# Optimization experiments

Hardware: AMD Instinct MI355X
Metric: run time of the kernel (lower is better)

The kernel has to match this reference:

```python
import jax, jax.numpy as jnp
import numpy as np

D_IN = 1024
D_OUT = 1024
NUM_HEADS = 16
HEAD_DIM = D_OUT // NUM_HEADS


def setup_inputs() -> dict:
    key = jax.random.key(0)
    kx, kq, kk, kv, ko = jax.random.split(key, 5)
    s = 1.0 / np.sqrt(D_IN)
    return {
        "x": jax.random.normal(kx, (1, 4096, D_IN), dtype=jnp.float32),
        "Wq": jax.random.normal(kq, (D_IN, D_OUT), dtype=jnp.float32) * s,
        "Wk": jax.random.normal(kk, (D_IN, D_OUT), dtype=jnp.float32) * s,
        "Wv": jax.random.normal(kv, (D_IN, D_OUT), dtype=jnp.float32) * s,
        "Wo": jax.random.normal(ko, (D_OUT, D_OUT), dtype=jnp.float32) * s,
    }


def reference(x, Wq, Wk, Wv, Wo):
    b, s, _ = x.shape
    # project and split heads: [b, h, s, d]
    def split_heads(t):
        return t.reshape(b, s, NUM_HEADS, HEAD_DIM).transpose(0, 2, 1, 3)
    Q = split_heads(x @ Wq)
    K = split_heads(x @ Wk)
    V = split_heads(x @ Wv)
    scores = jnp.einsum("bhqd,bhkd->bhqk", Q, K) / jnp.sqrt(jnp.float32(HEAD_DIM))
    causal = jnp.triu(jnp.ones((s, s), dtype=bool), k=1)  # True above diagonal
    scores = jnp.where(causal, -jnp.inf, scores)
    probs = jax.nn.softmax(scores, axis=-1)
    out = jnp.einsum("bhqk,bhkd->bhqd", probs, V)
    out = out.transpose(0, 2, 1, 3).reshape(b, s, D_OUT)
    return out @ Wo
```

## Files before the change

kernel.cpp:

```cpp
#include <hip/hip_runtime.h>
#include <cstdint>

#define S_LEN 4096
#define D_MODEL 1024
#define NHEAD 16
#define HDIM 64

typedef __bf16 bf16_t;
typedef __bf16 bf16x8 __attribute__((ext_vector_type(8)));
typedef __bf16 bf16x4 __attribute__((ext_vector_type(4)));
typedef float floatx4 __attribute__((ext_vector_type(4)));

#define QSCALE 0.18033688011112042f

__device__ __forceinline__ void lds_cp16(void* lds, const void* g) {
    __builtin_amdgcn_global_load_lds(
        (const __attribute__((address_space(1))) unsigned int*)g,
        (__attribute__((address_space(3))) unsigned int*)lds,
        16, 0, 0);
}

__device__ __forceinline__ float fast_exp2(float x) {
    float r;
    asm("v_exp_f32 %0, %1" : "=v"(r) : "v"(x));
    return r;
}

__global__ __launch_bounds__(256) void k_prep(const float* __restrict__ x,
                                              const float* __restrict__ Wq,
                                              const float* __restrict__ Wk,
                                              const float* __restrict__ Wv,
                                              const float* __restrict__ Wo,
                                              bf16_t* __restrict__ xb,
                                              bf16_t* __restrict__ WtQKV,
                                              bf16_t* __restrict__ WtO) {
    const int bx = blockIdx.x;
    if (bx < 4096) {
        int i = bx * 256 + threadIdx.x;
        float4 v = ((const float4*)x)[i];
        bf16x4 o;
        o[0] = (bf16_t)v.x; o[1] = (bf16_t)v.y; o[2] = (bf16_t)v.z; o[3] = (bf16_t)v.w;
        *(bf16x4*)(xb + (size_t)i * 4) = o;
        return;
    }
    __shared__ float lds[64][65];
    const int i = bx - 4096;
    const int z = i >> 8, rem = i & 255;
    const float* W = (z == 0) ? Wq : (z == 1) ? Wk : (z == 2) ? Wv : Wo;
    bf16_t* Wt = (z < 3) ? (WtQKV + (size_t)z * 1048576) : WtO;
    const int k0 = (rem >> 4) * 64, n0 = (rem & 15) * 64;
    const int t = threadIdx.x, cl = t & 63, rl = t >> 6;
#pragma unroll
    for (int r = 0; r < 16; ++r)
        lds[r * 4 + rl][cl] = W[(size_t)(k0 + r * 4 + rl) * 1024 + n0 + cl];
    __syncthreads();
#pragma unroll
    for (int r = 0; r < 16; ++r)
        Wt[(size_t)(n0 + r * 4 + rl) * 1024 + k0 + cl] = (bf16_t)lds[cl][r * 4 + rl];
}

template <int MODE, int MT>
__global__ __launch_bounds__(256) void k_gemm(const bf16_t* __restrict__ A,
                                              const bf16_t* __restrict__ Bt,
                                              float* __restrict__ Cout,
                                              bf16_t* __restrict__ Qb,
                                              bf16_t* __restrict__ Kb,
                                              bf16_t* __restrict__ Vt) {
    constexpr int MI = MT / 32;
    __shared__ __align__(16) bf16_t sA[MT * 32];
    __shared__ __align__(16) bf16_t sB[128 * 32];
    const int t = threadIdx.x, w = t >> 6, lane = t & 63, quad = lane >> 4, l15 = lane & 15;
    const int m0 = blockIdx.x * MT, n0 = blockIdx.y * 128;
    const int wm = w >> 1, wn = w & 1;

    floatx4 acc[MI][4];
#pragma unroll
    for (int i = 0; i < MI; ++i)
#pragma unroll
        for (int j = 0; j < 4; ++j)
            acc[i][j] = floatx4{0.f, 0.f, 0.f, 0.f};

    for (int kb = 0; kb < 32; ++kb) {
        __syncthreads();
#pragma unroll
        for (int r = 0; r < MT / 64; ++r) {
            int c = t + 256 * r;
            int row = c >> 2, kq = c & 3;
            lds_cp16(&sA[w * 512 + r * 2048],
                     A + (size_t)(m0 + row) * 1024 + kb * 32 + kq * 8);
        }
#pragma unroll
        for (int r = 0; r < 2; ++r) {
            int c = t + 256 * r;
            int row = c >> 2, kq = c & 3;
            lds_cp16(&sB[w * 512 + r * 2048],
                     Bt + (size_t)(n0 + row) * 1024 + kb * 32 + kq * 8);
        }
        __syncthreads();
        bf16x8 af[MI], bfr[4];
#pragma unroll
        for (int i = 0; i < MI; ++i)
            af[i] = *(const bf16x8*)&sA[(wm * (MT / 2) + i * 16 + l15) * 32 + quad * 8];
#pragma unroll
        for (int j = 0; j < 4; ++j)
            bfr[j] = *(const bf16x8*)&sB[(wn * 64 + j * 16 + l15) * 32 + quad * 8];
#pragma unroll
        for (int i = 0; i < MI; ++i)
#pragma unroll
            for (int j = 0; j < 4; ++j)
                acc[i][j] = __builtin_amdgcn_mfma_f32_16x16x32_bf16(af[i], bfr[j],
                                                                    acc[i][j], 0, 0, 0);
    }

    const int mrow = m0 + wm * (MT / 2) + quad * 4;
    if (MODE == 0) {
        const int ncol = n0 + wn * 64 + l15;
#pragma unroll
        for (int i = 0; i < MI; ++i)
#pragma unroll
            for (int j = 0; j < 4; ++j)
#pragma unroll
                for (int r = 0; r < 4; ++r)
                    Cout[(size_t)(mrow + i * 16 + r) * 1024 + ncol + j * 16] = acc[i][j][r];
    } else {
        const int g = (int)blockIdx.y >> 3;
        const int ncbase = ((int)blockIdx.y & 7) * 128 + wn * 64 + l15;
        if (g == 2) {
#pragma unroll
            for (int j = 0; j < 4; ++j) {
                int nc = ncbase + j * 16;
                int hh = nc >> 6, dd = nc & 63;
                bf16_t* dst = Vt + (size_t)hh * 262144 + (size_t)dd * 64;
#pragma unroll
                for (int i = 0; i < MI; ++i) {
                    int s0r = mrow + i * 16;
                    bf16x4 pk;
                    pk[0] = (bf16_t)acc[i][j][0]; pk[1] = (bf16_t)acc[i][j][1];
                    pk[2] = (bf16_t)acc[i][j][2]; pk[3] = (bf16_t)acc[i][j][3];
                    int kk = s0r & 63;
                    int pp = (kk & 0x20) | ((kk & 0xC) << 1) | ((kk & 0x10) >> 2);
                    *(bf16x4*)&dst[(size_t)(s0r >> 6) * 4096 + pp] = pk;
                }
            }
        } else {
            bf16_t* base = g ? Kb : Qb;
            const float sc = g ? 1.0f : QSCALE;
#pragma unroll
            for (int j = 0; j < 4; ++j) {
                int nc = ncbase + j * 16;
                int hh = nc >> 6, dd = nc & 63;
#pragma unroll
                for (int i = 0; i < MI; ++i)
#pragma unroll
                    for (int r = 0; r < 4; ++r)
                        base[(size_t)hh * 262144 + (size_t)(mrow + i * 16 + r) * 64 + dd] =
                            (bf16_t)(acc[i][j][r] * sc);
            }
        }
    }
}

__global__ __launch_bounds__(256, 4) void k_attn(const bf16_t* __restrict__ Qb,
                                                 const bf16_t* __restrict__ Kb,
                                                 const bf16_t* __restrict__ Vt,
                                                 bf16_t* __restrict__ OP0,
                                                 bf16_t* __restrict__ OP1,
                                                 float* __restrict__ Lp) {
    __shared__ __align__(16) bf16_t Ks[2][64 * 64];
    __shared__ __align__(16) bf16_t Vts[2][64 * 64];
    const int bid = blockIdx.x;
    const int slot = bid >> 8, jj = bid & 255, g = jj >> 5, u = jj & 31;
    const int h = u >> 1, sp = u & 1;
    const int qb = (slot == 0) ? (31 - g) : (slot == 1) ? (16 + g)
                 : (slot == 2) ? (15 - g) : g;
    const int t = threadIdx.x, w = t >> 6, quad = (t & 63) >> 4, l15 = t & 15;
    const bf16_t* Qh = Qb + (size_t)h * 262144;
    const bf16_t* Kh = Kb + (size_t)h * 262144;
    const bf16_t* Vth = Vt + (size_t)h * 262144;

    const bf16_t* Qrow = Qh + (size_t)(qb * 128 + w * 32 + l15) * 64;
    bf16x8 bq[2][2];
#pragma unroll
    for (int qt = 0; qt < 2; ++qt)
#pragma unroll
        for (int kh = 0; kh < 2; ++kh)
            bq[qt][kh] = *(const bf16x8*)(Qrow + qt * 1024 + kh * 32 + quad * 8);

    bf16x8 vones;
#pragma unroll
    for (int e = 0; e < 8; ++e) vones[e] = (bf16_t)1.0f;

    floatx4 lacc[2];
    floatx4 o_acc[2][4];
#pragma unroll
    for (int qt = 0; qt < 2; ++qt) {
        lacc[qt] = floatx4{0.f, 0.f, 0.f, 0.f};
#pragma unroll
        for (int j = 0; j < 4; ++j) o_acc[qt][j] = floatx4{0.f, 0.f, 0.f, 0.f};
    }

#define STAGE_K(b, kb_)                                                            \
    {                                                                              \
        _Pragma("unroll") for (int r = 0; r < 2; ++r) {                            \
            int c = t + 256 * r;                                                   \
            int row = c >> 3, sw = (c & 7) ^ (row & 7);                            \
            lds_cp16(&Ks[b][c * 8], Kh + (size_t)(kb_) * 4096 + row * 64 + sw * 8);\
        }                                                                          \
    }
#define STAGE_V(b, kb_)                                                            \
    {                                                                              \
        _Pragma("unroll") for (int r = 0; r < 2; ++r) {                            \
            int c = t + 256 * r;                                                   \
            int row = c >> 3, sw = (c & 7) ^ (row & 7);                            \
            lds_cp16(&Vts[b][c * 8], Vth + (size_t)(kb_) * 4096 + row * 64 + sw * 8);\
        }                                                                          \
    }

    const int t0 = sp ? (qb + 1) : 0;
    const int nIter = qb + 1;
    const int qmax = qb * 128 + w * 32 + 31;

    STAGE_K(0, t0)
    STAGE_V(0, t0)
    for (int it = 0; it < nIter; ++it) {
        const int kb = t0 + it;
        const int buf = it & 1;
        __syncthreads();
        if (it + 1 < nIter) {
            STAGE_K(buf ^ 1, kb + 1)
            STAGE_V(buf ^ 1, kb + 1)
        }
        const bool active = (kb * 64 <= qmax);

        if (active) {
            floatx4 st[2][4];
            __builtin_amdgcn_s_setprio(1);
#pragma unroll
            for (int j = 0; j < 4; ++j) {
                int rk = j * 16 + l15;
                bf16x8 a0 = *(const bf16x8*)&Ks[buf][rk * 64 + ((quad ^ (rk & 7)) * 8)];
                bf16x8 a1 = *(const bf16x8*)&Ks[buf][rk * 64 + (((quad + 4) ^ (rk & 7)) * 8)];
#pragma unroll
                for (int qt = 0; qt < 2; ++qt) {
                    floatx4 z = {0.f, 0.f, 0.f, 0.f};
                    st[qt][j] = __builtin_amdgcn_mfma_f32_16x16x32_bf16(a0, bq[qt][0], z, 0, 0, 0);
                    st[qt][j] = __builtin_amdgcn_mfma_f32_16x16x32_bf16(a1, bq[qt][1], st[qt][j], 0, 0, 0);
                }
            }
            __builtin_amdgcn_s_setprio(0);
            if (kb >= 2 * qb) {
#pragma unroll
                for (int qt = 0; qt < 2; ++qt) {
                    int qg = qb * 128 + w * 32 + qt * 16 + l15;
#pragma unroll
                    for (int j = 0; j < 4; ++j)
#pragma unroll
                        for (int r = 0; r < 4; ++r) {
                            int keyg = kb * 64 + j * 16 + quad * 4 + r;
                            if (keyg > qg) st[qt][j][r] = -1e30f;
                        }
                }
            }
            bf16x8 pa[2][2];
#pragma unroll
            for (int qt = 0; qt < 2; ++qt) {
#pragma unroll
                for (int j = 0; j < 4; ++j) {
                    st[qt][j][0] = fast_exp2(st[qt][j][0]);
                    st[qt][j][1] = fast_exp2(st[qt][j][1]);
                    st[qt][j][2] = fast_exp2(st[qt][j][2]);
                    st[qt][j][3] = fast_exp2(st[qt][j][3]);
                }
#pragma unroll
                for (int kh = 0; kh < 2; ++kh)
#pragma unroll
                    for (int m = 0; m < 4; ++m) {
                        pa[qt][kh][m]     = (bf16_t)st[qt][2 * kh][m];
                        pa[qt][kh][4 + m] = (bf16_t)st[qt][2 * kh + 1][m];
                    }
            }
            __builtin_amdgcn_s_setprio(1);
#pragma unroll
            for (int kh = 0; kh < 2; ++kh) {
                int pc = kh * 4 + quad;
#pragma unroll
                for (int j = 0; j < 4; ++j) {
                    int rd = j * 16 + l15;
                    bf16x8 bv = *(const bf16x8*)&Vts[buf][rd * 64 + ((pc ^ (rd & 7)) * 8)];
                    o_acc[0][j] = __builtin_amdgcn_mfma_f32_16x16x32_bf16(pa[0][kh], bv, o_acc[0][j], 0, 0, 0);
                    o_acc[1][j] = __builtin_amdgcn_mfma_f32_16x16x32_bf16(pa[1][kh], bv, o_acc[1][j], 0, 0, 0);
                }
                lacc[0] = __builtin_amdgcn_mfma_f32_16x16x32_bf16(pa[0][kh], vones, lacc[0], 0, 0, 0);
                lacc[1] = __builtin_amdgcn_mfma_f32_16x16x32_bf16(pa[1][kh], vones, lacc[1], 0, 0, 0);
            }
            __builtin_amdgcn_s_setprio(0);
        }
    }
    bf16_t* OPx = sp ? OP1 : OP0;
#pragma unroll
    for (int qt = 0; qt < 2; ++qt) {
        if (l15 == 0)
            *(floatx4*)&Lp[sp * 65536 + h * 4096 + qb * 128 + w * 32 + qt * 16 + quad * 4] =
                lacc[qt];
#pragma unroll
        for (int r = 0; r < 4; ++r) {
            int rowg = qb * 128 + w * 32 + qt * 16 + quad * 4 + r;
#pragma unroll
            for (int j = 0; j < 4; ++j)
                OPx[(size_t)rowg * 1024 + h * 64 + j * 16 + l15] = (bf16_t)o_acc[qt][j][r];
        }
    }
#undef STAGE_K
#undef STAGE_V
}

__global__ __launch_bounds__(256) void k_combine(const bf16_t* __restrict__ OP0,
                                                 const bf16_t* __restrict__ OP1,
                                                 const float* __restrict__ Lp,
                                                 bf16_t* __restrict__ Ob) {
    int gi = (blockIdx.x * 256 + threadIdx.x) * 4;
    int q = gi >> 10, hh = (gi & 1023) >> 6;
    float inv = 1.0f / (Lp[hh * 4096 + q] + Lp[65536 + hh * 4096 + q]);
    bf16x4 a = *(const bf16x4*)(OP0 + gi);
    bf16x4 b = *(const bf16x4*)(OP1 + gi);
    bf16x4 o;
#pragma unroll
    for (int r = 0; r < 4; ++r)
        o[r] = (bf16_t)(((float)a[r] + (float)b[r]) * inv);
    *(bf16x4*)(Ob + gi) = o;
}

extern "C" void kernel_launch(void* const* d_in, const int* in_sizes, int n_in,
                              void* d_out, int out_size, void* d_ws, size_t ws_size,
                              hipStream_t stream) {
    const float* x  = (const float*)d_in[0];
    const float* Wq = (const float*)d_in[1];
    const float* Wk = (const float*)d_in[2];
    const float* Wv = (const float*)d_in[3];
    const float* Wo = (const float*)d_in[4];

    bf16_t* ws = (bf16_t*)d_ws;
    bf16_t* Xb    = ws;
    bf16_t* WtQKV = Xb + 4194304;
    bf16_t* WtO   = WtQKV + 3145728;
    bf16_t* Qb    = WtO + 1048576;
    bf16_t* Kb    = Qb + 4194304;
    bf16_t* Vt    = Kb + 4194304;
    bf16_t* Ob    = Vt + 4194304;
    bf16_t* OP1   = Ob + 4194304;
    bf16_t* OP0   = Xb;
    float*  Lp    = (float*)WtQKV;
    float* out = (float*)d_out;

    k_prep<<<5120, 256, 0, stream>>>(x, Wq, Wk, Wv, Wo, Xb, WtQKV, WtO);
    k_gemm<1, 128><<<dim3(32, 24), 256, 0, stream>>>(Xb, WtQKV, nullptr, Qb, Kb, Vt);
    k_attn<<<1024, 256, 0, stream>>>(Qb, Kb, Vt, OP0, OP1, Lp);
    k_combine<<<4096, 256, 0, stream>>>(OP0, OP1, Lp, Ob);
    k_gemm<0, 64><<<dim3(64, 8), 256, 0, stream>>>(Ob, WtO, out, nullptr, nullptr, nullptr);
}
```

Measured before the change: 180.7 us.

## Split long causal query blocks into three KV chunks for better load balance

Reworks the causal attention work split so that the longer query blocks (qb>=16) are divided into three key-range partitions instead of two. Short blocks are packed via lookup tables into two extra slots, and the grid grows from 1024 to 1280 blocks. A third partial-output buffer and row-sum set are written, and the combine kernel adds them for the upper half of rows. The aim is to even out per-block work and reduce tail imbalance, at the cost of more partial-output traffic and extra combine reads.

```diff
diff --git a/kernel.cpp b/kernel.cpp
--- a/kernel.cpp
+++ b/kernel.cpp
@@ -165,14 +165,37 @@
                                                  const bf16_t* __restrict__ Vt,
                                                  bf16_t* __restrict__ OP0,
                                                  bf16_t* __restrict__ OP1,
+                                                 bf16_t* __restrict__ OP2,
                                                  float* __restrict__ Lp) {
     __shared__ __align__(16) bf16_t Ks[2][64 * 64];
     __shared__ __align__(16) bf16_t Vts[2][64 * 64];
     const int bid = blockIdx.x;
-    const int slot = bid >> 8, jj = bid & 255, g = jj >> 5, u = jj & 31;
-    const int h = u >> 1, sp = u & 1;
-    const int qb = (slot == 0) ? (31 - g) : (slot == 1) ? (16 + g)
-                 : (slot == 2) ? (15 - g) : g;
+    const int slot = bid >> 8, jj = bid & 255;
+    const int u = jj & 31, h = u >> 1;
+    const int gp = ((jj >> 5) << 1) | (u & 1);
+
+    int qb, part, c0, c1;
+    if (slot == 0) {
+        qb = 31 - gp; part = 0;
+        c0 = 0; c1 = (2 * qb + 4) / 3;
+    } else if (slot <= 2) {
+        qb = 16 + gp;
+        int L = 2 * qb + 2, p0 = (L + 2) / 3, p1 = (L - p0 + 1) / 2;
+        part = slot;
+        c0 = (slot == 1) ? p0 : p0 + p1;
+        c1 = (slot == 1) ? p0 + p1 : L;
+    } else {
+        if (slot == 3) {
+            qb = (int)((0xaabb77ccdd99eeffULL >> (4 * gp)) & 15);
+            part = gp & 1;
+        } else {
+            qb = (int)((0x0101662323884545ULL >> (4 * gp)) & 15);
+            part = (0xCB2C >> gp) & 1;
+        }
+        c0 = part ? (qb + 1) : 0;
+        c1 = part ? (2 * qb + 2) : (qb + 1);
+    }
+
     const int t = threadIdx.x, w = t >> 6, quad = (t & 63) >> 4, l15 = t & 15;
     const bf16_t* Qh = Qb + (size_t)h * 262144;
     const bf16_t* Kh = Kb + (size_t)h * 262144;
@@ -216,14 +239,13 @@
         }                                                                          \
     }
 
-    const int t0 = sp ? (qb + 1) : 0;
-    const int nIter = qb + 1;
+    const int nIter = c1 - c0;
     const int qmax = qb * 128 + w * 32 + 31;
 
-    STAGE_K(0, t0)
-    STAGE_V(0, t0)
+    STAGE_K(0, c0)
+    STAGE_V(0, c0)
     for (int it = 0; it < nIter; ++it) {
-        const int kb = t0 + it;
+        const int kb = c0 + it;
         const int buf = it & 1;
         __syncthreads();
         if (it + 1 < nIter) {
@@ -296,18 +318,20 @@
             __builtin_amdgcn_s_setprio(0);
         }
     }
-    bf16_t* OPx = sp ? OP1 : OP0;
+    bf16_t* OPx = (part == 0) ? OP0 : (part == 1) ? OP1 : OP2;
+    const int rsub = (part == 2) ? 2048 : 0;
 #pragma unroll
     for (int qt = 0; qt < 2; ++qt) {
         if (l15 == 0)
-            *(floatx4*)&Lp[sp * 65536 + h * 4096 + qb * 128 + w * 32 + qt * 16 + quad * 4] =
+            *(floatx4*)&Lp[part * 65536 + h * 4096 + qb * 128 + w * 32 + qt * 16 + quad * 4] =
                 lacc[qt];
 #pragma unroll
         for (int r = 0; r < 4; ++r) {
             int rowg = qb * 128 + w * 32 + qt * 16 + quad * 4 + r;
 #pragma unroll
             for (int j = 0; j < 4; ++j)
-                OPx[(size_t)rowg * 1024 + h * 64 + j * 16 + l15] = (bf16_t)o_acc[qt][j][r];
+                OPx[(size_t)(rowg - rsub) * 1024 + h * 64 + j * 16 + l15] =
+                    (bf16_t)o_acc[qt][j][r];
         }
     }
 #undef STAGE_K
@@ -316,17 +340,26 @@
 
 __global__ __launch_bounds__(256) void k_combine(const bf16_t* __restrict__ OP0,
                                                  const bf16_t* __restrict__ OP1,
+                                                 const bf16_t* __restrict__ OP2,
                                                  const float* __restrict__ Lp,
                                                  bf16_t* __restrict__ Ob) {
     int gi = (blockIdx.x * 256 + threadIdx.x) * 4;
     int q = gi >> 10, hh = (gi & 1023) >> 6;
-    float inv = 1.0f / (Lp[hh * 4096 + q] + Lp[65536 + hh * 4096 + q]);
+    float l = Lp[hh * 4096 + q] + Lp[65536 + hh * 4096 + q];
+    float s2[4] = {0.f, 0.f, 0.f, 0.f};
+    if (q >= 2048) {
+        l += Lp[131072 + hh * 4096 + q];
+        bf16x4 c = *(const bf16x4*)(OP2 + (size_t)(gi - 2048 * 1024));
+#pragma unroll
+        for (int r = 0; r < 4; ++r) s2[r] = (float)c[r];
+    }
+    float inv = 1.0f / l;
     bf16x4 a = *(const bf16x4*)(OP0 + gi);
     bf16x4 b = *(const bf16x4*)(OP1 + gi);
     bf16x4 o;
 #pragma unroll
     for (int r = 0; r < 4; ++r)
-        o[r] = (bf16_t)(((float)a[r] + (float)b[r]) * inv);
+        o[r] = (bf16_t)(((float)a[r] + (float)b[r] + s2[r]) * inv);
     *(bf16x4*)(Ob + gi) = o;
 }
 
@@ -350,11 +383,12 @@
     bf16_t* OP1   = Ob + 4194304;
     bf16_t* OP0   = Xb;
     float*  Lp    = (float*)WtQKV;
+    bf16_t* OP2   = WtQKV + 393216;
     float* out = (float*)d_out;
 
     k_prep<<<5120, 256, 0, stream>>>(x, Wq, Wk, Wv, Wo, Xb, WtQKV, WtO);
     k_gemm<1, 128><<<dim3(32, 24), 256, 0, stream>>>(Xb, WtQKV, nullptr, Qb, Kb, Vt);
-    k_attn<<<1024, 256, 0, stream>>>(Qb, Kb, Vt, OP0, OP1, Lp);
-    k_combine<<<4096, 256, 0, stream>>>(OP0, OP1, Lp, Ob);
+    k_attn<<<1280, 256, 0, stream>>>(Qb, Kb, Vt, OP0, OP1, OP2, Lp);
+    k_combine<<<4096, 256, 0, stream>>>(OP0, OP1, OP2, Lp, Ob);
     k_gemm<0, 64><<<dim3(64, 8), 256, 0, stream>>>(Ob, WtO, out, nullptr, nullptr, nullptr);
 }
```

Result: no change. 182.3 us (+0.8%).

## Fuse split-KV combine into attention via last-arriver atomic counter

Applied to the files above, without the earlier changes.

Removes the separate combine kernel. Each attention block atomically increments a per-(head, query-block) counter after writing its partial output and row sums. The second block to arrive reads the other split's partial and writes the normalized bf16 output directly, using its own accumulators still held in registers. This saves one launch and one full read/write pass over the partial buffers. It adds a threadfence plus an atomic per block, and reuses the output buffer as scratch for the counters, which are zeroed in the prep kernel.

```diff
diff --git a/kernel.cpp b/kernel.cpp
--- a/kernel.cpp
+++ b/kernel.cpp
@@ -33,7 +33,8 @@
                                               const float* __restrict__ Wo,
                                               bf16_t* __restrict__ xb,
                                               bf16_t* __restrict__ WtQKV,
-                                              bf16_t* __restrict__ WtO) {
+                                              bf16_t* __restrict__ WtO,
+                                              unsigned int* __restrict__ cnt) {
     const int bx = blockIdx.x;
     if (bx < 4096) {
         int i = bx * 256 + threadIdx.x;
@@ -42,6 +43,10 @@
         o[0] = (bf16_t)v.x; o[1] = (bf16_t)v.y; o[2] = (bf16_t)v.z; o[3] = (bf16_t)v.w;
         *(bf16x4*)(xb + (size_t)i * 4) = o;
         return;
+    }
+    if (bx == 4096) {
+        cnt[threadIdx.x] = 0u;
+        cnt[threadIdx.x + 256] = 0u;
     }
     __shared__ float lds[64][65];
     const int i = bx - 4096;
@@ -165,9 +170,12 @@
                                                  const bf16_t* __restrict__ Vt,
                                                  bf16_t* __restrict__ OP0,
                                                  bf16_t* __restrict__ OP1,
-                                                 float* __restrict__ Lp) {
+                                                 float* __restrict__ Lp,
+                                                 bf16_t* __restrict__ Ob,
+                                                 unsigned int* __restrict__ cnt) {
     __shared__ __align__(16) bf16_t Ks[2][64 * 64];
     __shared__ __align__(16) bf16_t Vts[2][64 * 64];
+    __shared__ int slast;
     const int bid = blockIdx.x;
     const int slot = bid >> 8, jj = bid & 255, g = jj >> 5, u = jj & 31;
     const int h = u >> 1, sp = u & 1;
@@ -310,24 +318,30 @@
                 OPx[(size_t)rowg * 1024 + h * 64 + j * 16 + l15] = (bf16_t)o_acc[qt][j][r];
         }
     }
+    __threadfence();
+    __syncthreads();
+    if (t == 0) slast = (int)atomicAdd(&cnt[h * 32 + qb], 1u);
+    __syncthreads();
+    if (slast == 1) {
+        __threadfence();
+        const bf16_t* OPo = sp ? OP0 : OP1;
+        const float* Lpo = Lp + (sp ? 0 : 65536);
+#pragma unroll
+        for (int qt = 0; qt < 2; ++qt)
+#pragma unroll
+            for (int r = 0; r < 4; ++r) {
+                int rowg = qb * 128 + w * 32 + qt * 16 + quad * 4 + r;
+                float inv = __builtin_amdgcn_rcpf(lacc[qt][r] + Lpo[h * 4096 + rowg]);
+#pragma unroll
+                for (int j = 0; j < 4; ++j) {
+                    float other = (float)OPo[(size_t)rowg * 1024 + h * 64 + j * 16 + l15];
+                    Ob[(size_t)rowg * 1024 + h * 64 + j * 16 + l15] =
+                        (bf16_t)((o_acc[qt][j][r] + other) * inv);
+                }
+            }
+    }
 #undef STAGE_K
 #undef STAGE_V
-}
-
-__global__ __launch_bounds__(256) void k_combine(const bf16_t* __restrict__ OP0,
-                                                 const bf16_t* __restrict__ OP1,
-                                                 const float* __restrict__ Lp,
-                                                 bf16_t* __restrict__ Ob) {
-    int gi = (blockIdx.x * 256 + threadIdx.x) * 4;
-    int q = gi >> 10, hh = (gi & 1023) >> 6;
-    float inv = 1.0f / (Lp[hh * 4096 + q] + Lp[65536 + hh * 4096 + q]);
-    bf16x4 a = *(const bf16x4*)(OP0 + gi);
-    bf16x4 b = *(const bf16x4*)(OP1 + gi);
-    bf16x4 o;
-#pragma unroll
-    for (int r = 0; r < 4; ++r)
-        o[r] = (bf16_t)(((float)a[r] + (float)b[r]) * inv);
-    *(bf16x4*)(Ob + gi) = o;
 }
 
 extern "C" void kernel_launch(void* const* d_in, const int* in_sizes, int n_in,
@@ -351,10 +365,10 @@
     bf16_t* OP0   = Xb;
     float*  Lp    = (float*)WtQKV;
     float* out = (float*)d_out;
-
-    k_prep<<<5120, 256, 0, stream>>>(x, Wq, Wk, Wv, Wo, Xb, WtQKV, WtO);
+    unsigned int* cnt = (unsigned int*)d_out;
+
+    k_prep<<<5120, 256, 0, stream>>>(x, Wq, Wk, Wv, Wo, Xb, WtQKV, WtO, cnt);
     k_gemm<1, 128><<<dim3(32, 24), 256, 0, stream>>>(Xb, WtQKV, nullptr, Qb, Kb, Vt);
-    k_attn<<<1024, 256, 0, stream>>>(Qb, Kb, Vt, OP0, OP1, Lp);
-    k_combine<<<4096, 256, 0, stream>>>(OP0, OP1, Lp, Ob);
+    k_attn<<<1024, 256, 0, stream>>>(Qb, Kb, Vt, OP0, OP1, Lp, Ob, cnt);
     k_gemm<0, 64><<<dim3(64, 8), 256, 0, stream>>>(Ob, WtO, out, nullptr, nullptr, nullptr);
 }
```

Result: slower. 440.3 us (+143.6%).

## Double attention query tile to 256 rows with 512-thread blocks

Applied to the files above, without the earlier changes.

The attention kernel now uses 8 waves per block, covering 256 query rows instead of 128, and launches 512 blocks of 512 threads. Each staged K/V tile is shared by twice as many query rows, which halves LDS staging traffic per query and gives each thread a single 16-byte copy per tile. In exchange, causally masked waves in a block sit idle for more iterations, fewer blocks make scheduling coarser, and launch bounds change occupancy.

```diff
diff --git a/kernel.cpp b/kernel.cpp
--- a/kernel.cpp
+++ b/kernel.cpp
@@ -160,7 +160,7 @@
     }
 }
 
-__global__ __launch_bounds__(256, 4) void k_attn(const bf16_t* __restrict__ Qb,
+__global__ __launch_bounds__(512, 2) void k_attn(const bf16_t* __restrict__ Qb,
                                                  const bf16_t* __restrict__ Kb,
                                                  const bf16_t* __restrict__ Vt,
                                                  bf16_t* __restrict__ OP0,
@@ -169,16 +169,15 @@
     __shared__ __align__(16) bf16_t Ks[2][64 * 64];
     __shared__ __align__(16) bf16_t Vts[2][64 * 64];
     const int bid = blockIdx.x;
-    const int slot = bid >> 8, jj = bid & 255, g = jj >> 5, u = jj & 31;
+    const int grp = bid >> 8, jj = bid & 255, g = jj >> 5, u = jj & 31;
     const int h = u >> 1, sp = u & 1;
-    const int qb = (slot == 0) ? (31 - g) : (slot == 1) ? (16 + g)
-                 : (slot == 2) ? (15 - g) : g;
+    const int qp = grp ? g : (15 - g);
     const int t = threadIdx.x, w = t >> 6, quad = (t & 63) >> 4, l15 = t & 15;
     const bf16_t* Qh = Qb + (size_t)h * 262144;
     const bf16_t* Kh = Kb + (size_t)h * 262144;
     const bf16_t* Vth = Vt + (size_t)h * 262144;
 
-    const bf16_t* Qrow = Qh + (size_t)(qb * 128 + w * 32 + l15) * 64;
+    const bf16_t* Qrow = Qh + (size_t)(qp * 256 + w * 32 + l15) * 64;
     bf16x8 bq[2][2];
 #pragma unroll
     for (int qt = 0; qt < 2; ++qt)
@@ -201,24 +200,18 @@
 
 #define STAGE_K(b, kb_)                                                            \
     {                                                                              \
-        _Pragma("unroll") for (int r = 0; r < 2; ++r) {                            \
-            int c = t + 256 * r;                                                   \
-            int row = c >> 3, sw = (c & 7) ^ (row & 7);                            \
-            lds_cp16(&Ks[b][c * 8], Kh + (size_t)(kb_) * 4096 + row * 64 + sw * 8);\
-        }                                                                          \
+        int row = t >> 3, sw = (t & 7) ^ (row & 7);                                \
+        lds_cp16(&Ks[b][t * 8], Kh + (size_t)(kb_) * 4096 + row * 64 + sw * 8);    \
     }
 #define STAGE_V(b, kb_)                                                            \
     {                                                                              \
-        _Pragma("unroll") for (int r = 0; r < 2; ++r) {                            \
-            int c = t + 256 * r;                                                   \
-            int row = c >> 3, sw = (c & 7) ^ (row & 7);                            \
-            lds_cp16(&Vts[b][c * 8], Vth + (size_t)(kb_) * 4096 + row * 64 + sw * 8);\
-        }                                                                          \
-    }
-
-    const int t0 = sp ? (qb + 1) : 0;
-    const int nIter = qb + 1;
-    const int qmax = qb * 128 + w * 32 + 31;
+        int row = t >> 3, sw = (t & 7) ^ (row & 7);                                \
+        lds_cp16(&Vts[b][t * 8], Vth + (size_t)(kb_) * 4096 + row * 64 + sw * 8);  \
+    }
+
+    const int t0 = sp ? (2 * qp + 2) : 0;
+    const int nIter = 2 * qp + 2;
+    const int qmax = qp * 256 + w * 32 + 31;
 
     STAGE_K(0, t0)
     STAGE_V(0, t0)
@@ -248,10 +241,10 @@
                 }
             }
             __builtin_amdgcn_s_setprio(0);
-            if (kb >= 2 * qb) {
+            if (kb >= 4 * qp) {
 #pragma unroll
                 for (int qt = 0; qt < 2; ++qt) {
-                    int qg = qb * 128 + w * 32 + qt * 16 + l15;
+                    int qg = qp * 256 + w * 32 + qt * 16 + l15;
 #pragma unroll
                     for (int j = 0; j < 4; ++j)
 #pragma unroll
@@ -300,11 +293,11 @@
 #pragma unroll
     for (int qt = 0; qt < 2; ++qt) {
         if (l15 == 0)
-            *(floatx4*)&Lp[sp * 65536 + h * 4096 + qb * 128 + w * 32 + qt * 16 + quad * 4] =
+            *(floatx4*)&Lp[sp * 65536 + h * 4096 + qp * 256 + w * 32 + qt * 16 + quad * 4] =
                 lacc[qt];
 #pragma unroll
         for (int r = 0; r < 4; ++r) {
-            int rowg = qb * 128 + w * 32 + qt * 16 + quad * 4 + r;
+            int rowg = qp * 256 + w * 32 + qt * 16 + quad * 4 + r;
 #pragma unroll
             for (int j = 0; j < 4; ++j)
                 OPx[(size_t)rowg * 1024 + h * 64 + j * 16 + l15] = (bf16_t)o_acc[qt][j][r];
@@ -354,7 +347,7 @@
 
     k_prep<<<5120, 256, 0, stream>>>(x, Wq, Wk, Wv, Wo, Xb, WtQKV, WtO);
     k_gemm<1, 128><<<dim3(32, 24), 256, 0, stream>>>(Xb, WtQKV, nullptr, Qb, Kb, Vt);
-    k_attn<<<1024, 256, 0, stream>>>(Qb, Kb, Vt, OP0, OP1, Lp);
+    k_attn<<<512, 512, 0, stream>>>(Qb, Kb, Vt, OP0, OP1, Lp);
     k_combine<<<4096, 256, 0, stream>>>(OP0, OP1, Lp, Ob);
     k_gemm<0, 64><<<dim3(64, 8), 256, 0, stream>>>(Ob, WtO, out, nullptr, nullptr, nullptr);
 }
```

After: 186.2 us. 3.0% more time.
